# Performance work log

Measured on AMD Instinct MI355X. Metric: run time of the kernel, lower is better.

Reference implementation:

```python
import jax, jax.numpy as jnp
import numpy as np

T = 1024
B = 64
A = 128
ABSTRACT_PENALTY = 0.5
CONSISTENCY_RATIO = 1.0
NEG = -1e30  # acts as log(0) mask; exp underflows to exactly 0 in logsumexp
STOP_IX, CONT_IX = 0, 1


def setup_inputs() -> dict:
    key = jax.random.key(0)
    k1, k2, k3, k4, k5 = jax.random.split(key, 5)
    actions = jax.random.randint(k1, (T,), 0, A, dtype=jnp.int32)
    action_logps = jax.nn.log_softmax(jax.random.normal(k2, (T + 1, B, A), dtype=jnp.float32), axis=-1)
    stop_logps = jax.nn.log_softmax(jax.random.normal(k3, (T + 1, B, 2), dtype=jnp.float32), axis=-1)
    start_logps = jax.nn.log_softmax(jax.random.normal(k4, (T + 1, B), dtype=jnp.float32), axis=-1)
    consistency_penalties = -0.1 * jnp.abs(jax.random.normal(k5, (T + 1, T + 1, B), dtype=jnp.float32))
    return {
        'actions': actions,
        'action_logps': action_logps,
        'stop_logps': stop_logps,
        'start_logps': start_logps,
        'consistency_penalties': consistency_penalties,
    }


def _hsmm_loss(actions, action_logps, stop_logps, start_logps, consistency_penalties):
    T_ = actions.shape[0]
    b = start_logps.shape[1]
    # option_step_dist as fixed (T, b) buffer, rows > current step masked to NEG
    dist0 = jnp.full((T_, b), NEG, dtype=action_logps.dtype).at[0].set(start_logps[0])
    # step i=0: only the action logp (no stop/start rearrange, no consistency pen)
    logp0 = jax.nn.logsumexp(dist0 + action_logps[0, :, actions[0]][None, :])

    idx = jnp.arange(1, T_)
    stop_lps = stop_logps[1:T_, :, STOP_IX]          # (T-1, b)
    cont_lps = stop_logps[1:T_, :, CONT_IX]          # (T-1, b)
    start_lps = start_logps[1:T_]                    # (T-1, b)
    act_lps = action_logps[idx, :, actions[1:]]      # (T-1, b)
    # column i of consistency_penalties, rows :T (masked dist rows kill rows > i)
    cons_cols = jnp.transpose(consistency_penalties[:T_, 1:T_, :], (1, 0, 2))  # (T-1, T, b)

    def step(carry, xs):
        dist, logp, cons = carry
        i, stop_lp, cont_lp, start_lp, act_lp, cp = xs
        total_rearrange = jax.nn.logsumexp(dist + stop_lp[None, :]) - ABSTRACT_PENALTY
        new_mass = start_lp + total_rearrange
        dist = (dist + cont_lp[None, :]).at[i].set(new_mass)
        cons = cons + jax.nn.logsumexp(dist + cp)
        logp = logp + jax.nn.logsumexp(dist + act_lp[None, :])
        return (dist, logp, cons), None

    init = (dist0, logp0, jnp.zeros((), dist0.dtype))
    (dist, logp, cons), _ = jax.lax.scan(step, init, (idx, stop_lps, cont_lps, start_lps, act_lps, cons_cols))
    total_logp = logp + jax.nn.logsumexp(dist + stop_logps[T_, :, STOP_IX][None, :])
    return -total_logp + CONSISTENCY_RATIO * cons


def reference(actions, action_logps, stop_logps, start_logps, consistency_penalties):
    return _hsmm_loss(actions, action_logps, stop_logps, start_logps, consistency_penalties)
```

## Files before the change

kernel.cpp:

```cpp
#include <hip/hip_runtime.h>

#define T_N 1024
#define B_N 64
#define A_N 128
#define TP1 1025

typedef float f32x4 __attribute__((ext_vector_type(4)));

__device__ __forceinline__ float bcf(int x){ return __builtin_bit_cast(float, x); }
__device__ __forceinline__ int   bci(float x){ return __builtin_bit_cast(int, x); }

template<int CTRL, int RM>
__device__ __forceinline__ float dpp_add_step(float x){
  int t = __builtin_amdgcn_update_dpp(0, bci(x), CTRL, RM, 0xf, true);
  return x + bcf(t);
}
__device__ __forceinline__ float wave_sum64(float x){
  x = dpp_add_step<0x111,0xf>(x);
  x = dpp_add_step<0x112,0xf>(x);
  x = dpp_add_step<0x114,0xf>(x);
  x = dpp_add_step<0x118,0xf>(x);
  x = dpp_add_step<0x142,0xa>(x);
  x = dpp_add_step<0x143,0xc>(x);
  return bcf(__builtin_amdgcn_readlane(bci(x), 63));
}
__device__ __forceinline__ void wave_sum64_x4(float a, float b, float c, float d,
                                              float& ra, float& rb, float& rc, float& rd){
  a = dpp_add_step<0x111,0xf>(a); b = dpp_add_step<0x111,0xf>(b);
  c = dpp_add_step<0x111,0xf>(c); d = dpp_add_step<0x111,0xf>(d);
  a = dpp_add_step<0x112,0xf>(a); b = dpp_add_step<0x112,0xf>(b);
  c = dpp_add_step<0x112,0xf>(c); d = dpp_add_step<0x112,0xf>(d);
  a = dpp_add_step<0x114,0xf>(a); b = dpp_add_step<0x114,0xf>(b);
  c = dpp_add_step<0x114,0xf>(c); d = dpp_add_step<0x114,0xf>(d);
  a = dpp_add_step<0x118,0xf>(a); b = dpp_add_step<0x118,0xf>(b);
  c = dpp_add_step<0x118,0xf>(c); d = dpp_add_step<0x118,0xf>(d);
  a = dpp_add_step<0x142,0xa>(a); b = dpp_add_step<0x142,0xa>(b);
  c = dpp_add_step<0x142,0xa>(c); d = dpp_add_step<0x142,0xa>(d);
  a = dpp_add_step<0x143,0xc>(a); b = dpp_add_step<0x143,0xc>(b);
  c = dpp_add_step<0x143,0xc>(c); d = dpp_add_step<0x143,0xc>(d);
  ra = bcf(__builtin_amdgcn_readlane(bci(a), 63));
  rb = bcf(__builtin_amdgcn_readlane(bci(b), 63));
  rc = bcf(__builtin_amdgcn_readlane(bci(c), 63));
  rd = bcf(__builtin_amdgcn_readlane(bci(d), 63));
}
__device__ __forceinline__ float group16_sum(float x){
  x = dpp_add_step<0x111,0xf>(x);
  x = dpp_add_step<0x112,0xf>(x);
  x = dpp_add_step<0x114,0xf>(x);
  x = dpp_add_step<0x118,0xf>(x);
  return x;
}
template<int CTRL, int RM>
__device__ __forceinline__ float dpp_max_step(float x){
  int t = __builtin_amdgcn_update_dpp(bci(-3.4e38f), bci(x), CTRL, RM, 0xf, false);
  return fmaxf(x, bcf(t));
}
__device__ __forceinline__ float wave_max64(float x){
  x = dpp_max_step<0x111,0xf>(x);
  x = dpp_max_step<0x112,0xf>(x);
  x = dpp_max_step<0x114,0xf>(x);
  x = dpp_max_step<0x118,0xf>(x);
  x = dpp_max_step<0x142,0xa>(x);
  x = dpp_max_step<0x143,0xc>(x);
  return bcf(__builtin_amdgcn_readlane(bci(x), 63));
}

__global__ __launch_bounds__(256) void prep_kernel(
    const float* __restrict__ stop_logps,
    const float* __restrict__ start_logps,
    float* __restrict__ quadQ,
    float* __restrict__ cs,
    float* __restrict__ A1p)
{
  const int tid  = (int)threadIdx.x;
  const int lane = tid & 63;
  const int wv   = tid >> 6;
  const int p    = (int)blockIdx.x * 4 + wv;
  const float KAPPA = 0.60653065971263342f;
  const float2* stop2 = (const float2*)stop_logps;

  int g = (int)blockIdx.x * 256 + tid;
  A1p[g] = 0.f; A1p[g + 16384] = 0.f; A1p[g + 32768] = 0.f; A1p[g + 49152] = 0.f;

  if (p < 255) {
    const int i1 = 4 * p + 1;
    float2 q1 = stop2[(i1 + 0) * B_N + lane];
    float2 q2 = stop2[(i1 + 1) * B_N + lane];
    float2 q3 = stop2[(i1 + 2) * B_N + lane];
    float2 q4 = stop2[(i1 + 3) * B_N + lane];
    float t1 = start_logps[(i1 + 0) * B_N + lane];
    float t2 = start_logps[(i1 + 1) * B_N + lane];
    float t3 = start_logps[(i1 + 2) * B_N + lane];
    float t4 = start_logps[(i1 + 3) * B_N + lane];
    float e1 = __expf(q1.x), c1 = __expf(q1.y), s1 = KAPPA * __expf(t1);
    float e2 = __expf(q2.x), c2 = __expf(q2.y), s2 = KAPPA * __expf(t2);
    float e3 = __expf(q3.x), c3 = __expf(q3.y), s3 = KAPPA * __expf(t3);
    float e4 = __expf(q4.x), c4 = __expf(q4.y), s4 = KAPPA * __expf(t4);

    float c21  = c2 * c1;
    float c321 = c3 * c21;
    float V1 = e1;
    float V2 = e2 * c1;
    float V3 = e3 * c21;
    float V4 = e4 * c321;

    float Cq = c4 * c321;
    float S1 = c4 * c3 * c2 * s1;
    float S2 = c4 * c3 * s2;
    float S3 = c4 * s3;
    float S4 = s4;

    float k21 = wave_sum64(e2 * s1);
    float k31 = wave_sum64(e3 * c2 * s1);
    float k32 = wave_sum64(e3 * s2);
    float k41 = wave_sum64(e4 * c3 * c2 * s1);
    float k42 = wave_sum64(e4 * c3 * s2);
    float k43 = wave_sum64(e4 * s3);

    f32x4* qs = (f32x4*)quadQ;
    size_t base = (size_t)p * 4 * 64 + lane;
    qs[base + 0 * 64] = (f32x4){V1, V2, V3, V4};
    qs[base + 1 * 64] = (f32x4){Cq, S1, S2, S3};
    qs[base + 2 * 64] = (f32x4){S4, k21, k31, k32};
    qs[base + 3 * 64] = (f32x4){k41, k42, k43, 0.f};
  }

  if (blockIdx.x < 16 && wv == 0) {
    int c = (int)blockIdx.x;
    float s = 0.f;
    for (int k = 1; k <= 64; ++k) {
      int i = 64 * c + k;
      if (i <= 1023) s += stop2[i * B_N + lane].y;
    }
    cs[c * B_N + lane] = s;
  }
}

__global__ __launch_bounds__(64, 1) void scan_kernel(
    const float* __restrict__ stop_logps,
    const float* __restrict__ start_logps,
    const float* __restrict__ quadQ,
    float* __restrict__ z_ws,
    float* __restrict__ r_ws,
    float* __restrict__ wexp)
{
  const int lane = threadIdx.x;
  const float2* stop2 = (const float2*)stop_logps;

  float2 sct0 = stop2[1021 * B_N + lane];
  float2 sct1 = stop2[1022 * B_N + lane];
  float2 sct2 = stop2[1023 * B_N + lane];
  float stt0 = start_logps[1021 * B_N + lane];
  float stt1 = start_logps[1022 * B_N + lane];
  float stt2 = start_logps[1023 * B_N + lane];

  float z = __expf(start_logps[lane]);

  const f32x4* qs = (const f32x4*)quadQ;

  f32x4 qb[8][4];
  #pragma unroll
  for (int q = 0; q < 8; ++q)
    #pragma unroll
    for (int s = 0; s < 4; ++s)
      qb[q][s] = qs[((size_t)q * 4 + s) * 64 + lane];

  for (int p0 = 0; p0 < 248; p0 += 8) {
    #pragma unroll
    for (int q = 0; q < 8; ++q) {
      const int p = p0 + q;
      f32x4 V = qb[q][0];
      f32x4 Z = qb[q][1];
      f32x4 W = qb[q][2];
      f32x4 X = qb[q][3];
      {
        const int pn = p + 8;
        #pragma unroll
        for (int s = 0; s < 4; ++s)
          qb[q][s] = qs[((size_t)pn * 4 + s) * 64 + lane];
      }

      float d1, d2, d3, d4;
      wave_sum64_x4(z * V.x, z * V.y, z * V.z, z * V.w, d1, d2, d3, d4);
      float r1 = d1;
      float r2 = __builtin_fmaf(W.y, r1, d2);
      float r3 = __builtin_fmaf(W.w, r2, __builtin_fmaf(W.z, r1, d3));
      float r4 = __builtin_fmaf(X.z, r3,
                 __builtin_fmaf(X.y, r2, __builtin_fmaf(X.x, r1, d4)));
      if (lane == 0) *(f32x4*)(r_ws + 4 * p) = (f32x4){r1, r2, r3, r4};

      z = __builtin_fmaf(r4, W.x,
          __builtin_fmaf(r3, Z.w,
          __builtin_fmaf(r2, Z.z,
          __builtin_fmaf(r1, Z.y, z * Z.x))));

      if (q == 7 && (p0 & 8)) {
        z_ws[(4 * p + 4) * B_N + lane] = z;
      }
      if ((q & 3) == 3) {
        int rb  = bci(r4);
        int e16 = ((rb >> 23) & 255) - 127;
        z = ldexpf(z, -e16);
        if (lane == 0) wexp[p >> 2] = (float)e16;
      }
    }
  }
  #pragma unroll
  for (int q = 0; q < 7; ++q) {
    f32x4 V = qb[q][0];
    f32x4 Z = qb[q][1];
    f32x4 W = qb[q][2];
    f32x4 X = qb[q][3];
    float d1, d2, d3, d4;
    wave_sum64_x4(z * V.x, z * V.y, z * V.z, z * V.w, d1, d2, d3, d4);
    float r1 = d1;
    float r2 = __builtin_fmaf(W.y, r1, d2);
    float r3 = __builtin_fmaf(W.w, r2, __builtin_fmaf(W.z, r1, d3));
    float r4 = __builtin_fmaf(X.z, r3,
               __builtin_fmaf(X.y, r2, __builtin_fmaf(X.x, r1, d4)));
    if (lane == 0) *(f32x4*)(r_ws + 4 * (248 + q)) = (f32x4){r1, r2, r3, r4};
    z = __builtin_fmaf(r4, W.x,
        __builtin_fmaf(r3, Z.w,
        __builtin_fmaf(r2, Z.z,
        __builtin_fmaf(r1, Z.y, z * Z.x))));
    if (q == 3) {
      int rb  = bci(r4);
      int e16 = ((rb >> 23) & 255) - 127;
      z = ldexpf(z, -e16);
      if (lane == 0) wexp[62] = (float)e16;
    }
  }
  const float KAPPA = 0.60653065971263342f;
  {
    float esw = __expf(sct0.x), ecw = __expf(sct0.y), sv = KAPPA * __expf(stt0);
    float r = wave_sum64(z * esw);
    z = __builtin_fmaf(sv, r, z * ecw);
    if (lane == 0) r_ws[1020] = r;
  }
  {
    float esw = __expf(sct1.x), ecw = __expf(sct1.y), sv = KAPPA * __expf(stt1);
    float r = wave_sum64(z * esw);
    z = __builtin_fmaf(sv, r, z * ecw);
    if (lane == 0) r_ws[1021] = r;
  }
  {
    float esw = __expf(sct2.x), ecw = __expf(sct2.y), sv = KAPPA * __expf(stt2);
    float r = wave_sum64(z * esw);
    z = __builtin_fmaf(sv, r, z * ecw);
    if (lane == 0) r_ws[1022] = r;
  }
}

__global__ __launch_bounds__(64) void post_kernel(
    const int* __restrict__ actions,
    const float* __restrict__ action_logps,
    const float* __restrict__ stop_logps,
    const float* __restrict__ start_logps,
    const float* __restrict__ z_ws,
    const float* __restrict__ r_ws,
    const float* __restrict__ wexp,
    const float* __restrict__ cs,
    float* __restrict__ u_ws,
    float* __restrict__ D_ws,
    float* __restrict__ out)
{
  const int w    = (int)blockIdx.x;
  const int lane = (int)threadIdx.x;
  const float LN2   = 0.69314718055994531f;
  const float KAPPA = 0.60653065971263342f;
  const float2* stop2 = (const float2*)stop_logps;

  float wl = (lane < 63) ? wexp[lane] : 0.f;

  float Pv = LN2 * wave_sum64((lane < 4 * w) ? wl : 0.f);
  float e0 = bcf(__builtin_amdgcn_readlane(bci(wl), 4 * w + 0));
  float e1 = bcf(__builtin_amdgcn_readlane(bci(wl), 4 * w + 1));
  float e2 = bcf(__builtin_amdgcn_readlane(bci(wl), 4 * w + 2));

  float C = 0.f;
  for (int ww = 0; ww < w; ++ww) C += cs[ww * B_N + lane];

  float z;
  if (w == 0) {
    z = __expf(start_logps[lane]);
    u_ws[lane] = start_logps[lane];
  } else {
    float em = bcf(__builtin_amdgcn_readlane(bci(wl), 4 * w - 1));
    z = ldexpf(z_ws[(64 * w) * B_N + lane], -(int)em);
  }

  for (int k = 1; k <= 64; ++k) {
    int i = 64 * w + k;
    if (i > 1023) break;
    float cont = stop2[i * B_N + lane].y;
    float stv  = start_logps[i * B_N + lane];
    float r    = r_ws[i - 1];
    C += cont;
    float ecw = __expf(cont);
    float sv  = KAPPA * __expf(stv);
    z = __builtin_fmaf(r, sv, ecw * z);
    float zs = wave_sum64(z);
    float R  = __logf(r) + Pv - 0.5f;
    u_ws[i * B_N + lane] = stv + R - C;
    D_ws[i * B_N + lane] = C - (__logf(zs) + Pv);
    if (k == 16)      { z = ldexpf(z, -(int)e0); Pv += LN2 * e0; }
    else if (k == 32) { z = ldexpf(z, -(int)e1); Pv += LN2 * e1; }
    else if (k == 48) { z = ldexpf(z, -(int)e2); Pv += LN2 * e2; }
  }

  if (w == 15) {
    float st0 = start_logps[lane];
    int   a0  = actions[0];
    float al0 = action_logps[lane * A_N + a0];
    float lp0 = __logf(wave_sum64(__expf(st0 + al0)));
    float stopT = stop_logps[(T_N * B_N + lane) * 2 + 0];
    float fin = __logf(wave_sum64(z * __expf(stopT))) + Pv;
    if (lane == 0) out[0] = -(lp0 + fin);
  }
}

__global__ __launch_bounds__(256) void cons_logp_kernel(
    const float* __restrict__ cons_pen,
    const float* __restrict__ u_ws,
    const float* __restrict__ D_ws,
    const int* __restrict__ actions,
    const float* __restrict__ action_logps,
    float* __restrict__ A1p,
    float* __restrict__ LQ)
{
  const int bid  = (int)blockIdx.x;
  const int tid  = (int)threadIdx.x;
  const int lane = tid & 63;
  const int wv   = tid >> 6;

  __shared__ float sm[4][64];
  __shared__ float sa[4][64];

  if (bid < 512) {
    const int bq  = (lane & 15) * 4;
    const int row = lane >> 4;
    #pragma unroll
    for (int t = 0; t < 2; ++t) {
      const int j = t ? (1023 - bid) : bid;
      const float4 u4 = *(const float4*)(u_ws + j * B_N + bq);
      float* dst = A1p + ((j & 63) << 10);
      for (int i0 = j + 4 * wv; i0 <= 1023; i0 += 16) {
        int i  = i0 + row;
        int iL = i > 1023 ? 1023 : i;
        f32x4 cp4 = __builtin_nontemporal_load(
            (const f32x4*)(cons_pen + ((size_t)j * TP1 + iL) * B_N + bq));
        float4 d4  = *(const float4*)(D_ws + (size_t)iL * B_N + bq);
        bool valid = (i >= 1) && (i <= 1023);
        float a0 = u4.x + d4.x + cp4.x;
        float a1 = u4.y + d4.y + cp4.y;
        float a2 = u4.z + d4.z + cp4.z;
        float a3 = u4.w + d4.w + cp4.w;
        a0 = valid ? a0 : -1e30f;
        a1 = valid ? a1 : -1e30f;
        a2 = valid ? a2 : -1e30f;
        a3 = valid ? a3 : -1e30f;
        float sred = (__expf(a0) + __expf(a1)) + (__expf(a2) + __expf(a3));
        sred = group16_sum(sred);
        if (((lane & 15) == 15) && valid) atomicAdd(dst + i, sred);
      }
    }
  } else {
    const int i = 1535 - bid;
    int   ai = actions[i];
    float av = action_logps[((size_t)i * B_N + lane) * A_N + ai];

    float mA = -1e30f, aA = 0.f, mB = -1e30f, aB = 0.f;
    for (int jj = wv; jj <= i; jj += 8) {
      float u0 = u_ws[jj * B_N + lane];
      int   j1 = jj + 4;
      float u1 = (j1 <= i) ? u_ws[j1 * B_N + lane] : -1e30f;
      float n0 = fmaxf(mA, u0);
      aA = aA * __expf(mA - n0) + __expf(u0 - n0);
      mA = n0;
      float n1 = fmaxf(mB, u1);
      aB = aB * __expf(mB - n1) + __expf(u1 - n1);
      mB = n1;
    }
    float m   = fmaxf(mA, mB);
    float acc = aA * __expf(mA - m) + aB * __expf(mB - m);

    sm[wv][lane] = m; sa[wv][lane] = acc;
    __syncthreads();
    if (wv == 0) {
      float m0 = sm[0][lane], m1 = sm[1][lane], m2 = sm[2][lane], m3 = sm[3][lane];
      float M2 = fmaxf(fmaxf(m0, m1), fmaxf(m2, m3));
      float A  = sa[0][lane] * __expf(m0 - M2) + sa[1][lane] * __expf(m1 - M2)
               + sa[2][lane] * __expf(m2 - M2) + sa[3][lane] * __expf(m3 - M2);
      float S  = M2 + __logf(A);
      float val = S + D_ws[(size_t)i * B_N + lane] + av;
      float mx  = wave_max64(val);
      float sum = wave_sum64(__expf(val - mx));
      if (lane == 0) LQ[i] = mx + __logf(sum);
    }
  }
}

__global__ __launch_bounds__(256) void finish_kernel(
    const float* __restrict__ A1p,
    const float* __restrict__ LQ,
    float* __restrict__ out)
{
  const int i = (int)blockIdx.x * 256 + (int)threadIdx.x;
  float v = 0.f;
  if (i >= 1 && i <= 1023) {
    float a = 0.f;
    #pragma unroll 8
    for (int p = 0; p < 64; ++p) a += A1p[(p << 10) + i];
    v = __logf(a) - LQ[i];
  }
  float ws = wave_sum64(v);
  __shared__ float sb[4];
  if ((threadIdx.x & 63) == 0) sb[threadIdx.x >> 6] = ws;
  __syncthreads();
  if (threadIdx.x == 0) atomicAdd(out, sb[0] + sb[1] + sb[2] + sb[3]);
}

extern "C" void kernel_launch(void* const* d_in, const int* in_sizes, int n_in,
                              void* d_out, int out_size, void* d_ws, size_t ws_size,
                              hipStream_t stream) {
  const int*   actions      = (const int*)d_in[0];
  const float* action_logps = (const float*)d_in[1];
  const float* stop_logps   = (const float*)d_in[2];
  const float* start_logps  = (const float*)d_in[3];
  const float* cons_pen     = (const float*)d_in[4];
  float* out = (float*)d_out;

  float* z_ws  = (float*)d_ws;
  float* u_ws  = z_ws + T_N * B_N;
  float* D_ws  = u_ws + T_N * B_N;
  float* A1p   = D_ws + T_N * B_N;
  float* r_ws  = A1p + 64 * 1024;
  float* wexp  = r_ws + T_N;
  float* LQ    = wexp + 64;
  float* cs    = LQ + T_N;
  float* quadQ = cs + 16 * B_N;

  hipLaunchKernelGGL(prep_kernel, dim3(64), dim3(256), 0, stream,
                     stop_logps, start_logps, quadQ, cs, A1p);
  hipLaunchKernelGGL(scan_kernel, dim3(1), dim3(64), 0, stream,
                     stop_logps, start_logps, quadQ, z_ws, r_ws, wexp);
  hipLaunchKernelGGL(post_kernel, dim3(16), dim3(64), 0, stream,
                     actions, action_logps, stop_logps, start_logps,
                     z_ws, r_ws, wexp, cs, u_ws, D_ws, out);
  hipLaunchKernelGGL(cons_logp_kernel, dim3(1535), dim3(256), 0, stream,
                     cons_pen, u_ws, D_ws, actions, action_logps, A1p, LQ);
  hipLaunchKernelGGL(finish_kernel, dim3(4), dim3(256), 0, stream,
                     A1p, LQ, out);
}
```

Baseline: 481.1 us.

## Precompute triangular solve in prep, shorten scan dependency chain, fuse finish kernel

The prep kernel now folds the per-quad 4x4 triangular recurrence into composed coefficients (m and T terms). This lets the serial scan compute the next state z directly from the wave sums, which shortens the latency-critical dependency chain in the single-wave scan. It also writes z checkpoints every 32 steps so the post kernel runs with 32 blocks instead of 16, and it drops the finish kernel by adding a last-block ticket reduction inside cons_logp_kernel. The prep kernel is relaunched as 256 single-wave blocks. The risks are a different floating-point rounding order and the correctness of the atomic ticket and fence.

```diff
diff --git a/kernel.cpp b/kernel.cpp
--- a/kernel.cpp
+++ b/kernel.cpp
@@ -65,25 +65,25 @@
   return bcf(__builtin_amdgcn_readlane(bci(x), 63));
 }
 
-__global__ __launch_bounds__(256) void prep_kernel(
+__global__ __launch_bounds__(64) void prep_kernel(
     const float* __restrict__ stop_logps,
     const float* __restrict__ start_logps,
     float* __restrict__ quadQ,
-    float* __restrict__ cs,
-    float* __restrict__ A1p)
+    float* __restrict__ cs32,
+    float* __restrict__ A1p,
+    int*   __restrict__ ticket)
 {
-  const int tid  = (int)threadIdx.x;
-  const int lane = tid & 63;
-  const int wv   = tid >> 6;
-  const int p    = (int)blockIdx.x * 4 + wv;
+  const int bid  = (int)blockIdx.x;
+  const int lane = (int)threadIdx.x;
   const float KAPPA = 0.60653065971263342f;
   const float2* stop2 = (const float2*)stop_logps;
 
-  int g = (int)blockIdx.x * 256 + tid;
+  int g = bid * 64 + lane;
   A1p[g] = 0.f; A1p[g + 16384] = 0.f; A1p[g + 32768] = 0.f; A1p[g + 49152] = 0.f;
-
-  if (p < 255) {
-    const int i1 = 4 * p + 1;
+  if (bid == 255 && lane == 0) *ticket = 0;
+
+  if (bid < 255) {
+    const int i1 = 4 * bid + 1;
     float2 q1 = stop2[(i1 + 0) * B_N + lane];
     float2 q2 = stop2[(i1 + 1) * B_N + lane];
     float2 q3 = stop2[(i1 + 2) * B_N + lane];
@@ -117,22 +117,32 @@
     float k42 = wave_sum64(e4 * c3 * s2);
     float k43 = wave_sum64(e4 * s3);
 
+    float m21 = k21, m32 = k32, m43 = k43;
+    float m31 = __builtin_fmaf(k32, k21, k31);
+    float m42 = __builtin_fmaf(k43, k32, k42);
+    float m41 = __builtin_fmaf(k43, m31, __builtin_fmaf(k42, k21, k41));
+
+    float T4 = S4;
+    float T3 = __builtin_fmaf(S4, m43, S3);
+    float T2 = __builtin_fmaf(S4, m42, __builtin_fmaf(S3, m32, S2));
+    float T1 = __builtin_fmaf(S4, m41,
+               __builtin_fmaf(S3, m31, __builtin_fmaf(S2, m21, S1)));
+
     f32x4* qs = (f32x4*)quadQ;
-    size_t base = (size_t)p * 4 * 64 + lane;
+    size_t base = (size_t)bid * 4 * 64 + lane;
     qs[base + 0 * 64] = (f32x4){V1, V2, V3, V4};
-    qs[base + 1 * 64] = (f32x4){Cq, S1, S2, S3};
-    qs[base + 2 * 64] = (f32x4){S4, k21, k31, k32};
-    qs[base + 3 * 64] = (f32x4){k41, k42, k43, 0.f};
-  }
-
-  if (blockIdx.x < 16 && wv == 0) {
-    int c = (int)blockIdx.x;
+    qs[base + 1 * 64] = (f32x4){Cq, T1, T2, T3};
+    qs[base + 2 * 64] = (f32x4){T4, m21, m31, m32};
+    qs[base + 3 * 64] = (f32x4){m41, m42, m43, 0.f};
+  }
+
+  if (bid < 32) {
     float s = 0.f;
-    for (int k = 1; k <= 64; ++k) {
-      int i = 64 * c + k;
+    for (int k = 1; k <= 32; ++k) {
+      int i = 32 * bid + k;
       if (i <= 1023) s += stop2[i * B_N + lane].y;
     }
-    cs[c * B_N + lane] = s;
+    cs32[bid * B_N + lane] = s;
   }
 }
 
@@ -182,31 +192,31 @@
 
       float d1, d2, d3, d4;
       wave_sum64_x4(z * V.x, z * V.y, z * V.z, z * V.w, d1, d2, d3, d4);
+
       float r1 = d1;
-      float r2 = __builtin_fmaf(W.y, r1, d2);
-      float r3 = __builtin_fmaf(W.w, r2, __builtin_fmaf(W.z, r1, d3));
-      float r4 = __builtin_fmaf(X.z, r3,
-                 __builtin_fmaf(X.y, r2, __builtin_fmaf(X.x, r1, d4)));
+      float r2 = __builtin_fmaf(W.y, d1, d2);
+      float r3 = __builtin_fmaf(W.w, d2, __builtin_fmaf(W.z, d1, d3));
+      float r4 = __builtin_fmaf(X.z, d3,
+                 __builtin_fmaf(X.y, d2, __builtin_fmaf(X.x, d1, d4)));
       if (lane == 0) *(f32x4*)(r_ws + 4 * p) = (f32x4){r1, r2, r3, r4};
 
-      z = __builtin_fmaf(r4, W.x,
-          __builtin_fmaf(r3, Z.w,
-          __builtin_fmaf(r2, Z.z,
-          __builtin_fmaf(r1, Z.y, z * Z.x))));
-
-      if (q == 7 && (p0 & 8)) {
-        z_ws[(4 * p + 4) * B_N + lane] = z;
-      }
+      float p1 = __builtin_fmaf(d2, Z.z, __builtin_fmaf(d1, Z.y, z * Z.x));
+      float p2 = __builtin_fmaf(d4, W.x, d3 * Z.w);
+      z = p1 + p2;
+
       if ((q & 3) == 3) {
         int rb  = bci(r4);
         int e16 = ((rb >> 23) & 255) - 127;
         z = ldexpf(z, -e16);
         if (lane == 0) wexp[p >> 2] = (float)e16;
+        if (q == 7)
+          z_ws[(4 * p + 4) * B_N + lane] = z;
       }
     }
   }
   #pragma unroll
   for (int q = 0; q < 7; ++q) {
+    const int p = 248 + q;
     f32x4 V = qb[q][0];
     f32x4 Z = qb[q][1];
     f32x4 W = qb[q][2];
@@ -214,15 +224,14 @@
     float d1, d2, d3, d4;
     wave_sum64_x4(z * V.x, z * V.y, z * V.z, z * V.w, d1, d2, d3, d4);
     float r1 = d1;
-    float r2 = __builtin_fmaf(W.y, r1, d2);
-    float r3 = __builtin_fmaf(W.w, r2, __builtin_fmaf(W.z, r1, d3));
-    float r4 = __builtin_fmaf(X.z, r3,
-               __builtin_fmaf(X.y, r2, __builtin_fmaf(X.x, r1, d4)));
-    if (lane == 0) *(f32x4*)(r_ws + 4 * (248 + q)) = (f32x4){r1, r2, r3, r4};
-    z = __builtin_fmaf(r4, W.x,
-        __builtin_fmaf(r3, Z.w,
-        __builtin_fmaf(r2, Z.z,
-        __builtin_fmaf(r1, Z.y, z * Z.x))));
+    float r2 = __builtin_fmaf(W.y, d1, d2);
+    float r3 = __builtin_fmaf(W.w, d2, __builtin_fmaf(W.z, d1, d3));
+    float r4 = __builtin_fmaf(X.z, d3,
+               __builtin_fmaf(X.y, d2, __builtin_fmaf(X.x, d1, d4)));
+    if (lane == 0) *(f32x4*)(r_ws + 4 * p) = (f32x4){r1, r2, r3, r4};
+    float p1 = __builtin_fmaf(d2, Z.z, __builtin_fmaf(d1, Z.y, z * Z.x));
+    float p2 = __builtin_fmaf(d4, W.x, d3 * Z.w);
+    z = p1 + p2;
     if (q == 3) {
       int rb  = bci(r4);
       int e16 = ((rb >> 23) & 255) - 127;
@@ -259,7 +268,7 @@
     const float* __restrict__ z_ws,
     const float* __restrict__ r_ws,
     const float* __restrict__ wexp,
-    const float* __restrict__ cs,
+    const float* __restrict__ cs32,
     float* __restrict__ u_ws,
     float* __restrict__ D_ws,
     float* __restrict__ out)
@@ -272,25 +281,22 @@
 
   float wl = (lane < 63) ? wexp[lane] : 0.f;
 
-  float Pv = LN2 * wave_sum64((lane < 4 * w) ? wl : 0.f);
-  float e0 = bcf(__builtin_amdgcn_readlane(bci(wl), 4 * w + 0));
-  float e1 = bcf(__builtin_amdgcn_readlane(bci(wl), 4 * w + 1));
-  float e2 = bcf(__builtin_amdgcn_readlane(bci(wl), 4 * w + 2));
+  float Pv = LN2 * wave_sum64((lane < 2 * w) ? wl : 0.f);
+  float e0 = bcf(__builtin_amdgcn_readlane(bci(wl), 2 * w));
 
   float C = 0.f;
-  for (int ww = 0; ww < w; ++ww) C += cs[ww * B_N + lane];
+  for (int c = 0; c < w; ++c) C += cs32[c * B_N + lane];
 
   float z;
   if (w == 0) {
     z = __expf(start_logps[lane]);
     u_ws[lane] = start_logps[lane];
   } else {
-    float em = bcf(__builtin_amdgcn_readlane(bci(wl), 4 * w - 1));
-    z = ldexpf(z_ws[(64 * w) * B_N + lane], -(int)em);
-  }
-
-  for (int k = 1; k <= 64; ++k) {
-    int i = 64 * w + k;
+    z = z_ws[(32 * w) * B_N + lane];
+  }
+
+  for (int k = 1; k <= 32; ++k) {
+    int i = 32 * w + k;
     if (i > 1023) break;
     float cont = stop2[i * B_N + lane].y;
     float stv  = start_logps[i * B_N + lane];
@@ -303,12 +309,10 @@
     float R  = __logf(r) + Pv - 0.5f;
     u_ws[i * B_N + lane] = stv + R - C;
     D_ws[i * B_N + lane] = C - (__logf(zs) + Pv);
-    if (k == 16)      { z = ldexpf(z, -(int)e0); Pv += LN2 * e0; }
-    else if (k == 32) { z = ldexpf(z, -(int)e1); Pv += LN2 * e1; }
-    else if (k == 48) { z = ldexpf(z, -(int)e2); Pv += LN2 * e2; }
-  }
-
-  if (w == 15) {
+    if (k == 16) { z = ldexpf(z, -(int)e0); Pv += LN2 * e0; }
+  }
+
+  if (w == 31) {
     float st0 = start_logps[lane];
     int   a0  = actions[0];
     float al0 = action_logps[lane * A_N + a0];
@@ -326,7 +330,9 @@
     const int* __restrict__ actions,
     const float* __restrict__ action_logps,
     float* __restrict__ A1p,
-    float* __restrict__ LQ)
+    float* __restrict__ LQ,
+    int*   __restrict__ ticket,
+    float* __restrict__ out)
 {
   const int bid  = (int)blockIdx.x;
   const int tid  = (int)threadIdx.x;
@@ -335,6 +341,8 @@
 
   __shared__ float sm[4][64];
   __shared__ float sa[4][64];
+  __shared__ float sb[4];
+  __shared__ int sdone;
 
   if (bid < 512) {
     const int bq  = (lane & 15) * 4;
@@ -398,26 +406,35 @@
       if (lane == 0) LQ[i] = mx + __logf(sum);
     }
   }
-}
-
-__global__ __launch_bounds__(256) void finish_kernel(
-    const float* __restrict__ A1p,
-    const float* __restrict__ LQ,
-    float* __restrict__ out)
-{
-  const int i = (int)blockIdx.x * 256 + (int)threadIdx.x;
-  float v = 0.f;
-  if (i >= 1 && i <= 1023) {
-    float a = 0.f;
-    #pragma unroll 8
-    for (int p = 0; p < 64; ++p) a += A1p[(p << 10) + i];
-    v = __logf(a) - LQ[i];
-  }
-  float ws = wave_sum64(v);
-  __shared__ float sb[4];
-  if ((threadIdx.x & 63) == 0) sb[threadIdx.x >> 6] = ws;
+
   __syncthreads();
-  if (threadIdx.x == 0) atomicAdd(out, sb[0] + sb[1] + sb[2] + sb[3]);
+  if (tid == 0) {
+    __threadfence();
+    int old = atomicAdd(ticket, 1);
+    sdone = (old == 1534) ? 1 : 0;
+  }
+  __syncthreads();
+  if (sdone) {
+    __threadfence();
+    float vsum = 0.f;
+    for (int rep = 0; rep < 4; ++rep) {
+      int i = rep * 256 + tid;
+      if (i >= 1 && i <= 1023) {
+        float a = 0.f;
+        #pragma unroll 8
+        for (int pq = 0; pq < 64; ++pq)
+          a += __hip_atomic_load(&A1p[(pq << 10) + i],
+                                 __ATOMIC_RELAXED, __HIP_MEMORY_SCOPE_AGENT);
+        float lq = __hip_atomic_load(&LQ[i],
+                                 __ATOMIC_RELAXED, __HIP_MEMORY_SCOPE_AGENT);
+        vsum += __logf(a) - lq;
+      }
+    }
+    float ws = wave_sum64(vsum);
+    if (lane == 0) sb[wv] = ws;
+    __syncthreads();
+    if (tid == 0) atomicAdd(out, sb[0] + sb[1] + sb[2] + sb[3]);
+  }
 }
 
 extern "C" void kernel_launch(void* const* d_in, const int* in_sizes, int n_in,
@@ -437,18 +454,18 @@
   float* r_ws  = A1p + 64 * 1024;
   float* wexp  = r_ws + T_N;
   float* LQ    = wexp + 64;
-  float* cs    = LQ + T_N;
-  float* quadQ = cs + 16 * B_N;
-
-  hipLaunchKernelGGL(prep_kernel, dim3(64), dim3(256), 0, stream,
-                     stop_logps, start_logps, quadQ, cs, A1p);
+  float* cs32  = LQ + T_N;
+  float* quadQ = cs32 + 32 * B_N;
+  int*   ticket = (int*)(quadQ + 256 * 4 * B_N * 4);
+
+  hipLaunchKernelGGL(prep_kernel, dim3(256), dim3(64), 0, stream,
+                     stop_logps, start_logps, quadQ, cs32, A1p, ticket);
   hipLaunchKernelGGL(scan_kernel, dim3(1), dim3(64), 0, stream,
                      stop_logps, start_logps, quadQ, z_ws, r_ws, wexp);
-  hipLaunchKernelGGL(post_kernel, dim3(16), dim3(64), 0, stream,
+  hipLaunchKernelGGL(post_kernel, dim3(32), dim3(64), 0, stream,
                      actions, action_logps, stop_logps, start_logps,
-                     z_ws, r_ws, wexp, cs, u_ws, D_ws, out);
+                     z_ws, r_ws, wexp, cs32, u_ws, D_ws, out);
   hipLaunchKernelGGL(cons_logp_kernel, dim3(1535), dim3(256), 0, stream,
-                     cons_pen, u_ws, D_ws, actions, action_logps, A1p, LQ);
-  hipLaunchKernelGGL(finish_kernel, dim3(4), dim3(256), 0, stream,
-                     A1p, LQ, out);
-}
+                     cons_pen, u_ws, D_ws, actions, action_logps, A1p, LQ,
+                     ticket, out);
+}
```

Result: slower. 507.0 us (+5.4%).
